# Performance work log

Hardware: AMD Instinct MI355X
Metric: run time of the kernel (lower is better)

## Reference

```python
import jax, jax.numpy as jnp
import numpy as np

B, T, C = 2, 2048, 2048
NH, NKV, HD = 16, 8, 256
SOFTCAP = 50.0
ROPE_BASE = 10000.0


def setup_inputs() -> dict:
    key = jax.random.key(0)
    ks = jax.random.split(key, 5)
    s = 0.02
    return {
        "X": jax.random.normal(ks[0], (B, T, C), dtype=jnp.float32),
        "Wq": jax.random.normal(ks[1], (C, NH * HD), dtype=jnp.float32) * s,
        "Wk": jax.random.normal(ks[2], (C, NKV * HD), dtype=jnp.float32) * s,
        "Wv": jax.random.normal(ks[3], (C, NKV * HD), dtype=jnp.float32) * s,
        "Wo": jax.random.normal(ks[4], (NH * HD, C), dtype=jnp.float32) * s,
    }


def _rotate_half(x):
    x1, x2 = x[..., : x.shape[-1] // 2], x[..., x.shape[-1] // 2 :]
    return jnp.concatenate((-x2, x1), axis=-1)


def _rope_cos_sin(t, head_dim, dtype):
    inv_freq = 1.0 / ROPE_BASE ** (
        jnp.arange(0, head_dim, 2, dtype=jnp.int32).astype(jnp.float32) / head_dim
    )  # [HD/2]
    pos = jnp.arange(t, dtype=jnp.float32)  # [T]
    freqs = pos[:, None] * inv_freq[None, :]  # [T, HD/2]
    emb = jnp.concatenate((freqs, freqs), axis=-1)  # [T, HD]
    # shape [1, 1, T, HD] to broadcast over (B, H, T, HD)
    return (
        jnp.cos(emb).astype(dtype)[None, None],
        jnp.sin(emb).astype(dtype)[None, None],
    )


def reference(X, Wq, Wk, Wv, Wo):
    b, t, c = X.shape
    n_rep = NH // NKV

    q = (X @ Wq).reshape(b, t, NH, HD).transpose(0, 2, 1, 3)   # [B,NH,T,HD]
    k = (X @ Wk).reshape(b, t, NKV, HD).transpose(0, 2, 1, 3)  # [B,NKV,T,HD]
    v = (X @ Wv).reshape(b, t, NKV, HD).transpose(0, 2, 1, 3)

    cos, sin = _rope_cos_sin(t, HD, X.dtype)
    q = q * cos + _rotate_half(q) * sin
    k = k * cos + _rotate_half(k) * sin

    # repeat_kv (GQA): [B,NKV,T,HD] -> [B,NH,T,HD]
    k = jnp.repeat(k, n_rep, axis=1)
    v = jnp.repeat(v, n_rep, axis=1)

    scale = 256.0 ** (-0.5)  # hardcoded in source
    att = jnp.einsum("bhqd,bhkd->bhqk", q, k) * scale
    # tanh logit softcapping
    att = SOFTCAP * jnp.tanh(att / SOFTCAP)
    # causal mask
    causal = jnp.tril(jnp.ones((t, t), dtype=bool))
    att = jnp.where(causal[None, None], att, -jnp.inf)
    att = jax.nn.softmax(att, axis=-1)

    y = jnp.einsum("bhqk,bhkd->bhqd", att, v)  # [B,NH,T,HD]
    y = y.transpose(0, 2, 1, 3).reshape(b, t, NH * HD)
    return y @ Wo
```

## Files before the change

### kernel.cpp

```cpp
#include <hip/hip_runtime.h>
#include <hip/hip_bf16.h>

#define NHD 16
#define NKVH 8
#define HDIM 256
#define TSEQ 2048
#define BATCH 2

typedef unsigned int   u32;
typedef unsigned short u16;

typedef __attribute__((ext_vector_type(8))) short bf16x8;
typedef __attribute__((ext_vector_type(4))) float floatx4;

__device__ inline u32 cvt2bf(float lo, float hi) {
  u32 r;
  asm("v_cvt_pk_bf16_f32 %0, %1, %2" : "=v"(r) : "v"(lo), "v"(hi));
  return r;
}
__device__ inline u16 f2bf(float f) {
  union { float f; u32 i; } v; v.f = f;
  u32 r = v.i + 0x7fffu + ((v.i >> 16) & 1u);
  return (u16)(r >> 16);
}
__device__ inline float bf2f(u16 u) {
  union { u32 i; float f; } v; v.i = ((u32)u) << 16; return v.f;
}
__device__ inline float fexp2(float x) {
  float r; asm("v_exp_f32 %0, %1" : "=v"(r) : "v"(x)); return r;
}
__device__ inline float frcp(float x) {
  float r; asm("v_rcp_f32 %0, %1" : "=v"(r) : "v"(x)); return r;
}

typedef const __attribute__((address_space(1))) u32* gptr_t;
typedef __attribute__((address_space(3))) u32* lptr_t;
__device__ inline void gl_lds16(const void* g, void* l) {
  __builtin_amdgcn_global_load_lds((gptr_t)g, (lptr_t)l, 16, 0, 0);
}

__device__ inline void tconv_body(const float* __restrict__ in,
                                  u16* __restrict__ out, int R, int Cc,
                                  int bx, int by, int tid) {
  __shared__ float tile[64][65];
  const int r0 = by * 64, c0 = bx * 64;
  const int tr = tid >> 4;
  const int tc = (tid & 15) * 4;
#pragma unroll
  for (int j = 0; j < 4; ++j) {
    float4 v = *(const float4*)(in + (size_t)(r0 + tr + j * 16) * Cc + c0 + tc);
    tile[tr + j * 16][tc + 0] = v.x;
    tile[tr + j * 16][tc + 1] = v.y;
    tile[tr + j * 16][tc + 2] = v.z;
    tile[tr + j * 16][tc + 3] = v.w;
  }
  __syncthreads();
#pragma unroll
  for (int j = 0; j < 4; ++j) {
    int c = tr + j * 16;
    u16 o[4];
#pragma unroll
    for (int i = 0; i < 4; ++i) o[i] = f2bf(tile[tc + i][c]);
    *(uint2*)(out + (size_t)(c0 + c) * R + r0 + tc) = *(const uint2*)o;
  }
}

__global__ __launch_bounds__(256) void tconv_k(
    const float* __restrict__ in, u16* __restrict__ out, int R, int Cc)
{
  tconv_body(in, out, R, Cc, blockIdx.x, blockIdx.y, threadIdx.x);
}

__global__ __launch_bounds__(256) void xconv_k(
    const float* __restrict__ in, u16* __restrict__ out)
{
  size_t i = (size_t)blockIdx.x * 256 + threadIdx.x;
  float4 a = *(const float4*)(in + i * 8);
  float4 b = *(const float4*)(in + i * 8 + 4);
  uint4 o;
  o.x = cvt2bf(a.x, a.y); o.y = cvt2bf(a.z, a.w);
  o.z = cvt2bf(b.x, b.y); o.w = cvt2bf(b.z, b.w);
  *(uint4*)(out + i * 8) = o;
}

__global__ __launch_bounds__(256) void prep_k(
    const float* __restrict__ X,  const float* __restrict__ Wq,
    const float* __restrict__ Wk, const float* __restrict__ Wv,
    u16* __restrict__ XB, u16* __restrict__ WqT, u16* __restrict__ WkvT)
{
  const int bid = blockIdx.x, tid = threadIdx.x;
  if (bid < 4096) {
    size_t i = (size_t)bid * 256 + tid;
    float4 a = *(const float4*)(X + i * 8);
    float4 b = *(const float4*)(X + i * 8 + 4);
    uint4 o;
    o.x = cvt2bf(a.x, a.y); o.y = cvt2bf(a.z, a.w);
    o.z = cvt2bf(b.x, b.y); o.w = cvt2bf(b.z, b.w);
    *(uint4*)(XB + i * 8) = o;
  } else if (bid < 6144) {
    int idx = bid - 4096;
    tconv_body(Wq, WqT, 2048, 4096, idx & 63, idx >> 6, tid);
  } else if (bid < 7168) {
    int idx = bid - 6144;
    tconv_body(Wk, WkvT, 2048, 2048, idx & 31, idx >> 5, tid);
  } else {
    int idx = bid - 7168;
    tconv_body(Wv, WkvT + (size_t)2048 * 2048, 2048, 2048, idx & 31, idx >> 5, tid);
  }
}

template<int EPI, int BM>
__global__ __launch_bounds__(512, 2) void gemm256_k(
    const u16* __restrict__ Ab, const u16* __restrict__ BTp,
    void* __restrict__ Op, int M, int N, int K)
{
  constexpr int NI = BM / 32;
  constexpr int AI = BM / 64;
  __shared__ u16 LA[2][BM * 64];
  __shared__ u16 LB[2][256 * 64];
  const int t = threadIdx.x;
  const int lane = t & 63, wave = t >> 6;
  const int lg = lane >> 4, l15 = lane & 15;
  const int wm = wave >> 2, wn = wave & 3;
  const int mtiles = M / BM;
  const int mt = (int)blockIdx.x % mtiles, nt = (int)blockIdx.x / mtiles;
  const int m0 = mt * BM, n0 = nt << 8;

  const int arow = wave * (BM / 8) + (lane >> 3);
  const int ska  = ((lane & 7) ^ (arow & 7)) << 3;
  const int brow = wave * 32 + (lane >> 3);
  const int skb  = ((lane & 7) ^ (brow & 7)) << 3;
  const u16* Ag = Ab  + (size_t)(m0 + arow) * K + ska;
  const u16* Bg = BTp + (size_t)(n0 + brow) * K + skb;

  auto STAGE = [&](int k0, int sel) {
#pragma unroll
    for (int q = 0; q < AI; ++q)
      gl_lds16(Ag + k0 + (size_t)q * 8 * K, &LA[sel][(wave * (BM / 8) + q * 8) * 64]);
#pragma unroll
    for (int q = 0; q < 4; ++q)
      gl_lds16(Bg + k0 + (size_t)q * 8 * K, &LB[sel][(wave * 32 + q * 8) * 64]);
  };

  floatx4 acc[NI][4];
#pragma unroll
  for (int i = 0; i < NI; ++i)
#pragma unroll
    for (int j = 0; j < 4; ++j) acc[i][j] = (floatx4){0.f, 0.f, 0.f, 0.f};

  STAGE(0, 0);
  const int KT = K >> 6;
  for (int kt = 0; kt < KT; ++kt) {
    const int sel = kt & 1;
    if (kt + 1 < KT) {
      STAGE((kt + 1) << 6, sel ^ 1);
      if constexpr (BM == 256) asm volatile("s_waitcnt vmcnt(8)" ::: "memory");
      else                     asm volatile("s_waitcnt vmcnt(6)" ::: "memory");
    } else {
      asm volatile("s_waitcnt vmcnt(0)" ::: "memory");
    }
    __builtin_amdgcn_s_barrier();
    __builtin_amdgcn_sched_barrier(0);
    __builtin_amdgcn_s_setprio(1);
#pragma unroll
    for (int ks = 0; ks < 2; ++ks) {
      const int c = (ks << 2) + lg;
      bf16x8 bfv[4];
#pragma unroll
      for (int j = 0; j < 4; ++j) {
        int row = wn * 64 + (j << 4) + l15;
        bfv[j] = *(const bf16x8*)(&LB[sel][row * 64 + ((c ^ (row & 7)) << 3)]);
      }
#pragma unroll
      for (int i = 0; i < NI; ++i) {
        int row = wm * (BM / 2) + (i << 4) + l15;
        bf16x8 af = *(const bf16x8*)(&LA[sel][row * 64 + ((c ^ (row & 7)) << 3)]);
#pragma unroll
        for (int j = 0; j < 4; ++j)
          acc[i][j] = __builtin_amdgcn_mfma_f32_16x16x32_bf16(af, bfv[j], acc[i][j], 0, 0, 0);
      }
    }
    __builtin_amdgcn_s_setprio(0);
    __builtin_amdgcn_s_barrier();
  }

#pragma unroll
  for (int i = 0; i < NI; ++i) {
#pragma unroll
    for (int j = 0; j < 4; ++j) {
#pragma unroll
      for (int r = 0; r < 4; ++r) {
        int m = m0 + wm * (BM / 2) + (i << 4) + (lg << 2) + r;
        int n = n0 + wn * 64 + (j << 4) + l15;
        float v = acc[i][j][r];
        int bb = m >> 11, tt = m & 2047;
        if (EPI == 0) {
          ((float*)Op)[(size_t)m * N + n] = v;
        } else if (EPI == 1) {
          int h = n >> 8, d = n & 255;
          ((u16*)Op)[(((size_t)bb * NHD + h) * TSEQ + tt) * HDIM + d] = f2bf(v);
        } else {
          if (n < 2048) {
            int h = n >> 8, d = n & 255;
            ((u16*)Op)[(((size_t)bb * NKVH + h) * TSEQ + tt) * HDIM + d] = f2bf(v);
          } else {
            int n2 = n - 2048;
            int h = n2 >> 8, d = n2 & 255;
            ((u16*)Op)[8388608u + (((size_t)bb * NKVH + h) * HDIM + d) * TSEQ + tt] = f2bf(v);
          }
        }
      }
    }
  }
}

__global__ __launch_bounds__(256) void rope_k(u16* Qb, u16* Kb) {
  size_t idx = (size_t)blockIdx.x * 256 + threadIdx.x;
  const size_t qtot = (size_t)BATCH * NHD * TSEQ * 128;
  u16* buf;
  if (idx < qtot) buf = Qb;
  else { idx -= qtot; buf = Kb; }
  int d = (int)(idx & 127);
  size_t rest = idx >> 7;
  int tt = (int)(rest & (TSEQ - 1));
  float invf = exp2f(-(float)d * 0.103810253f);
  float th = (float)tt * invf;
  float sn, cs;
  sincosf(th, &sn, &cs);
  size_t base = rest * HDIM;
  float x1 = bf2f(buf[base + d]);
  float x2 = bf2f(buf[base + d + 128]);
  buf[base + d]       = f2bf(x1 * cs - x2 * sn);
  buf[base + d + 128] = f2bf(x2 * cs + x1 * sn);
}

__global__ __launch_bounds__(256, 2) void attn_k(
    const u16* __restrict__ Q, const u16* __restrict__ Kb,
    const u16* __restrict__ Vt, u16* __restrict__ Y)
{
  __shared__ u16 Ks2[2][32 * 256];
  __shared__ u16 Vs2[2][256 * 32];
  __shared__ u16 Ps[4 * 16 * 32];
  __shared__ float Ls[4][16];
  const int t = threadIdx.x, lane = t & 63, w = t >> 6;
  const int lg = lane >> 4, l15 = lane & 15;
  const int qt = 31 - (int)blockIdx.y;
  const int h = (int)blockIdx.x >> 1, b = (int)blockIdx.x & 1;
  const int hkv = h >> 1;

  const u16* Kg = Kb + ((size_t)(b * NKVH + hkv)) * TSEQ * HDIM;
  const u16* Vg = Vt + ((size_t)(b * NKVH + hkv)) * HDIM * TSEQ;

  int koff[4], voff[4];
#pragma unroll
  for (int q = 0; q < 4; ++q) {
    int krow = w * 8 + q * 2 + (lane >> 5);
    int kcc  = lane & 31;
    koff[q] = krow * 256 + ((kcc ^ (krow & 7)) << 3);
    int vd  = w * 64 + q * 16 + (lane >> 2);
    voff[q] = vd * TSEQ + (((lane & 3) ^ ((vd >> 2) & 3)) << 3);
  }

  auto STAGE = [&](int st, int sel) {
    const u16* kbase = Kg + (size_t)st * (32 * 256);
    const u16* vbase = Vg + st * 32;
#pragma unroll
    for (int q = 0; q < 4; ++q)
      gl_lds16(kbase + koff[q], &Ks2[sel][(w * 8 + q * 2) * 256]);
#pragma unroll
    for (int q = 0; q < 4; ++q)
      gl_lds16(vbase + voff[q], &Vs2[sel][(w * 64 + q * 16) * 32]);
  };

  const u16* Qg = Q + (((size_t)(b * NHD + h)) * TSEQ + qt * 64 + w * 16 + l15) * HDIM;
  bf16x8 qf[8];
#pragma unroll
  for (int ks = 0; ks < 8; ++ks) qf[ks] = *(const bf16x8*)(Qg + ks * 32 + lg * 8);

  floatx4 accY[16];
#pragma unroll
  for (int i = 0; i < 16; ++i) accY[i] = (floatx4){0.f, 0.f, 0.f, 0.f};
  float rsum = 0.f;

  const int qglob = qt * 64 + w * 16 + l15;
  const int qmaxw = qt * 64 + w * 16 + 15;
  const int nst = 2 * qt + 2;
  const int fps = (l15 ^ (l15 >> 2)) & 3;

  STAGE(0, 0);
  for (int st = 0; st < nst; ++st) {
    const int sel = st & 1;
    if (st + 1 < nst) {
      STAGE(st + 1, sel ^ 1);
      asm volatile("s_waitcnt vmcnt(8)" ::: "memory");
    } else {
      asm volatile("s_waitcnt vmcnt(0)" ::: "memory");
    }
    __builtin_amdgcn_s_barrier();
    __builtin_amdgcn_sched_barrier(0);

    if (st * 32 <= qmaxw) {
      __builtin_amdgcn_s_setprio(1);
#pragma unroll
      for (int stile = 0; stile < 2; ++stile) {
        floatx4 sa0 = (floatx4){0.f, 0.f, 0.f, 0.f};
        floatx4 sa1 = (floatx4){0.f, 0.f, 0.f, 0.f};
#pragma unroll
        for (int ks = 0; ks < 8; ++ks) {
          int row = (stile << 4) + l15;
          int c = (ks << 2) + lg;
          bf16x8 kf = *(const bf16x8*)((const char*)Ks2[sel] +
                        row * 512 + ((c ^ (row & 7)) << 4));
          if (ks & 1)
            sa1 = __builtin_amdgcn_mfma_f32_16x16x32_bf16(kf, qf[ks], sa1, 0, 0, 0);
          else
            sa0 = __builtin_amdgcn_mfma_f32_16x16x32_bf16(kf, qf[ks], sa0, 0, 0, 0);
        }
        int sbase = st * 32 + (stile << 4) + (lg << 2);
        float p[4];
#pragma unroll
        for (int r = 0; r < 4; ++r) {
          float u = fexp2((sa0[r] + sa1[r]) * 0.0036067376f);
          float pv = fexp2(-144.26950408f * frcp(u + 1.0f));
          pv = (sbase + r <= qglob) ? pv : 0.0f;
          p[r] = pv;
          rsum += pv;
        }
        uint2 pw;
        pw.x = cvt2bf(p[0], p[1]);
        pw.y = cvt2bf(p[2], p[3]);
        int o = (stile << 5) + (lg << 3);
        int gran = (o >> 4) ^ fps;
        *(uint2*)((char*)Ps + (w << 10) + l15 * 64 + (gran << 4) + (o & 15)) = pw;
      }
      {
        bf16x8 pf = *(const bf16x8*)((const char*)Ps + (w << 10) + l15 * 64 +
                      ((lg ^ fps) << 4));
#pragma unroll
        for (int dt = 0; dt < 16; ++dt) {
          int row = (dt << 4) + l15;
          bf16x8 vf = *(const bf16x8*)((const char*)Vs2[sel] +
                        row * 64 + ((lg ^ ((row >> 2) & 3)) << 4));
          accY[dt] = __builtin_amdgcn_mfma_f32_16x16x32_bf16(pf, vf, accY[dt], 0, 0, 0);
        }
      }
      __builtin_amdgcn_s_setprio(0);
    }
    __builtin_amdgcn_s_barrier();
  }

  rsum += __shfl_xor(rsum, 16);
  rsum += __shfl_xor(rsum, 32);
  if (lane < 16) Ls[w][l15] = rsum;
  __syncthreads();
  float inv[4];
#pragma unroll
  for (int r = 0; r < 4; ++r) inv[r] = 1.0f / Ls[w][(lg << 2) + r];

  u16* Yg = Y + ((size_t)(b * TSEQ + qt * 64 + w * 16)) * (NHD * HDIM) + h * HDIM;
#pragma unroll
  for (int dt = 0; dt < 16; ++dt)
#pragma unroll
    for (int r = 0; r < 4; ++r)
      Yg[(size_t)((lg << 2) + r) * (NHD * HDIM) + (dt << 4) + l15] =
          f2bf(accY[dt][r] * inv[r]);
}

extern "C" void kernel_launch(void* const* d_in, const int* in_sizes, int n_in,
                              void* d_out, int out_size, void* d_ws, size_t ws_size,
                              hipStream_t stream) {
  const float* X  = (const float*)d_in[0];
  const float* Wq = (const float*)d_in[1];
  const float* Wk = (const float*)d_in[2];
  const float* Wv = (const float*)d_in[3];
  const float* Wo = (const float*)d_in[4];
  float* out = (float*)d_out;

  u16* ws = (u16*)d_ws;
  dim3 blk(256);

  if (ws_size >= (size_t)117440512) {
    u16* XB   = ws;
    u16* WqT  = ws + 8388608;
    u16* WkvT = ws + 16777216;
    u16* Qb   = ws + 25165824;
    u16* KVb  = ws + 41943040;
    u16* Yb   = ws;
    u16* WoT  = ws + 25165824;

    prep_k<<<dim3(8192), blk, 0, stream>>>(X, Wq, Wk, Wv, XB, WqT, WkvT);
    gemm256_k<1, 256><<<dim3(256), dim3(512), 0, stream>>>(XB, WqT,  Qb,  4096, 4096, 2048);
    gemm256_k<3, 256><<<dim3(256), dim3(512), 0, stream>>>(XB, WkvT, KVb, 4096, 4096, 2048);
    rope_k<<<dim3(49152), blk, 0, stream>>>(Qb, KVb);
    attn_k<<<dim3(32, 32), blk, 0, stream>>>(Qb, KVb, KVb + 8388608, Yb);
    tconv_k<<<dim3(32, 64), blk, 0, stream>>>(Wo, WoT, 4096, 2048);
    gemm256_k<0, 128><<<dim3(256), dim3(512), 0, stream>>>(Yb, WoT, out, 4096, 2048, 4096);
  } else {
    u16* XB   = ws;
    u16* WT   = ws + 8388608;
    u16* Qb   = ws + 16777216;
    u16* KVb  = ws + 33554432;
    u16* Yb   = ws;
    u16* WoT  = ws + 16777216;

    xconv_k<<<dim3(4096), blk, 0, stream>>>(X, XB);
    tconv_k<<<dim3(64, 32), blk, 0, stream>>>(Wq, WT, 2048, 4096);
    gemm256_k<1, 256><<<dim3(256), dim3(512), 0, stream>>>(XB, WT, Qb, 4096, 4096, 2048);
    tconv_k<<<dim3(32, 32), blk, 0, stream>>>(Wk, WT, 2048, 2048);
    tconv_k<<<dim3(32, 32), blk, 0, stream>>>(Wv, WT + (size_t)2048 * 2048, 2048, 2048);
    gemm256_k<3, 256><<<dim3(256), dim3(512), 0, stream>>>(XB, WT, KVb, 4096, 4096, 2048);
    rope_k<<<dim3(49152), blk, 0, stream>>>(Qb, KVb);
    attn_k<<<dim3(32, 32), blk, 0, stream>>>(Qb, KVb, KVb + 8388608, Yb);
    tconv_k<<<dim3(32, 64), blk, 0, stream>>>(Wo, WoT, 4096, 2048);
    gemm256_k<0, 128><<<dim3(256), dim3(512), 0, stream>>>(Yb, WoT, out, 4096, 2048, 4096);
  }
}
```

Baseline: 421.6 us.

## Process 128 query rows per attention block to reuse K/V tiles

Each wave now computes two 16-row query groups against every staged K/V tile, doubling the query tile per block and halving the grid. This halves global and LDS staging traffic of K/V per query row and reuses each K/V fragment read from LDS across two MFMAs. The cost is doubled accumulator registers, which risks spilling, and coarser causal work units with fewer blocks, which can hurt load balance.

```diff
diff --git a/kernel.cpp b/kernel.cpp
--- a/kernel.cpp
+++ b/kernel.cpp
@@ -234,17 +234,18 @@
   buf[base + d + 128] = f2bf(x2 * cs + x1 * sn);
 }
 
-__global__ __launch_bounds__(256, 2) void attn_k(
+__global__ __attribute__((amdgpu_waves_per_eu(2, 2))) __launch_bounds__(256)
+void attn_k(
     const u16* __restrict__ Q, const u16* __restrict__ Kb,
     const u16* __restrict__ Vt, u16* __restrict__ Y)
 {
   __shared__ u16 Ks2[2][32 * 256];
   __shared__ u16 Vs2[2][256 * 32];
-  __shared__ u16 Ps[4 * 16 * 32];
-  __shared__ float Ls[4][16];
+  __shared__ u16 Ps[4 * 32 * 32];
+  __shared__ float Ls[4][2][16];
   const int t = threadIdx.x, lane = t & 63, w = t >> 6;
   const int lg = lane >> 4, l15 = lane & 15;
-  const int qt = 31 - (int)blockIdx.y;
+  const int qt = 15 - (int)blockIdx.y;
   const int h = (int)blockIdx.x >> 1, b = (int)blockIdx.x & 1;
   const int hkv = h >> 1;
 
@@ -272,19 +273,27 @@
       gl_lds16(vbase + voff[q], &Vs2[sel][(w * 64 + q * 16) * 32]);
   };
 
-  const u16* Qg = Q + (((size_t)(b * NHD + h)) * TSEQ + qt * 64 + w * 16 + l15) * HDIM;
-  bf16x8 qf[8];
-#pragma unroll
-  for (int ks = 0; ks < 8; ++ks) qf[ks] = *(const bf16x8*)(Qg + ks * 32 + lg * 8);
-
-  floatx4 accY[16];
-#pragma unroll
-  for (int i = 0; i < 16; ++i) accY[i] = (floatx4){0.f, 0.f, 0.f, 0.f};
-  float rsum = 0.f;
-
-  const int qglob = qt * 64 + w * 16 + l15;
-  const int qmaxw = qt * 64 + w * 16 + 15;
-  const int nst = 2 * qt + 2;
+  bf16x8 qf[2][8];
+#pragma unroll
+  for (int g = 0; g < 2; ++g) {
+    const u16* Qg = Q + (((size_t)(b * NHD + h)) * TSEQ +
+                         qt * 128 + w * 32 + g * 16 + l15) * HDIM;
+#pragma unroll
+    for (int ks = 0; ks < 8; ++ks)
+      qf[g][ks] = *(const bf16x8*)(Qg + ks * 32 + lg * 8);
+  }
+
+  floatx4 accY[2][16];
+#pragma unroll
+  for (int g = 0; g < 2; ++g)
+#pragma unroll
+    for (int i = 0; i < 16; ++i) accY[g][i] = (floatx4){0.f, 0.f, 0.f, 0.f};
+  float rsum0 = 0.f, rsum1 = 0.f;
+
+  const int qg0 = qt * 128 + w * 32 + l15;
+  const int qg1 = qg0 + 16;
+  const int qmaxw = qt * 128 + w * 32 + 31;
+  const int nst = 4 * qt + 4;
   const int fps = (l15 ^ (l15 >> 2)) & 3;
 
   STAGE(0, 0);
@@ -306,42 +315,64 @@
         floatx4 sa0 = (floatx4){0.f, 0.f, 0.f, 0.f};
         floatx4 sa1 = (floatx4){0.f, 0.f, 0.f, 0.f};
 #pragma unroll
-        for (int ks = 0; ks < 8; ++ks) {
-          int row = (stile << 4) + l15;
-          int c = (ks << 2) + lg;
-          bf16x8 kf = *(const bf16x8*)((const char*)Ks2[sel] +
-                        row * 512 + ((c ^ (row & 7)) << 4));
-          if (ks & 1)
-            sa1 = __builtin_amdgcn_mfma_f32_16x16x32_bf16(kf, qf[ks], sa1, 0, 0, 0);
-          else
-            sa0 = __builtin_amdgcn_mfma_f32_16x16x32_bf16(kf, qf[ks], sa0, 0, 0, 0);
+        for (int kh = 0; kh < 2; ++kh) {
+          bf16x8 kf[4];
+#pragma unroll
+          for (int kk = 0; kk < 4; ++kk) {
+            int ks = kh * 4 + kk;
+            int row = (stile << 4) + l15;
+            int c = (ks << 2) + lg;
+            kf[kk] = *(const bf16x8*)((const char*)Ks2[sel] +
+                       row * 512 + ((c ^ (row & 7)) << 4));
+          }
+#pragma unroll
+          for (int kk = 0; kk < 4; ++kk) {
+            sa0 = __builtin_amdgcn_mfma_f32_16x16x32_bf16(kf[kk], qf[0][kh * 4 + kk], sa0, 0, 0, 0);
+            sa1 = __builtin_amdgcn_mfma_f32_16x16x32_bf16(kf[kk], qf[1][kh * 4 + kk], sa1, 0, 0, 0);
+          }
         }
         int sbase = st * 32 + (stile << 4) + (lg << 2);
-        float p[4];
-#pragma unroll
-        for (int r = 0; r < 4; ++r) {
-          float u = fexp2((sa0[r] + sa1[r]) * 0.0036067376f);
-          float pv = fexp2(-144.26950408f * frcp(u + 1.0f));
-          pv = (sbase + r <= qglob) ? pv : 0.0f;
-          p[r] = pv;
-          rsum += pv;
-        }
-        uint2 pw;
-        pw.x = cvt2bf(p[0], p[1]);
-        pw.y = cvt2bf(p[2], p[3]);
         int o = (stile << 5) + (lg << 3);
         int gran = (o >> 4) ^ fps;
-        *(uint2*)((char*)Ps + (w << 10) + l15 * 64 + (gran << 4) + (o & 15)) = pw;
+        {
+          float p[4];
+#pragma unroll
+          for (int r = 0; r < 4; ++r) {
+            float u = fexp2(sa0[r] * 0.0036067376f);
+            float pv = fexp2(-144.26950408f * frcp(u + 1.0f));
+            pv = (sbase + r <= qg0) ? pv : 0.0f;
+            p[r] = pv;
+            rsum0 += pv;
+          }
+          uint2 pw; pw.x = cvt2bf(p[0], p[1]); pw.y = cvt2bf(p[2], p[3]);
+          *(uint2*)((char*)Ps + (w << 11) + l15 * 64 + (gran << 4) + (o & 15)) = pw;
+        }
+        {
+          float p[4];
+#pragma unroll
+          for (int r = 0; r < 4; ++r) {
+            float u = fexp2(sa1[r] * 0.0036067376f);
+            float pv = fexp2(-144.26950408f * frcp(u + 1.0f));
+            pv = (sbase + r <= qg1) ? pv : 0.0f;
+            p[r] = pv;
+            rsum1 += pv;
+          }
+          uint2 pw; pw.x = cvt2bf(p[0], p[1]); pw.y = cvt2bf(p[2], p[3]);
+          *(uint2*)((char*)Ps + (w << 11) + (16 + l15) * 64 + (gran << 4) + (o & 15)) = pw;
+        }
       }
       {
-        bf16x8 pf = *(const bf16x8*)((const char*)Ps + (w << 10) + l15 * 64 +
-                      ((lg ^ fps) << 4));
+        bf16x8 pf0 = *(const bf16x8*)((const char*)Ps + (w << 11) +
+                       l15 * 64 + ((lg ^ fps) << 4));
+        bf16x8 pf1 = *(const bf16x8*)((const char*)Ps + (w << 11) +
+                       (16 + l15) * 64 + ((lg ^ fps) << 4));
 #pragma unroll
         for (int dt = 0; dt < 16; ++dt) {
           int row = (dt << 4) + l15;
           bf16x8 vf = *(const bf16x8*)((const char*)Vs2[sel] +
                         row * 64 + ((lg ^ ((row >> 2) & 3)) << 4));
-          accY[dt] = __builtin_amdgcn_mfma_f32_16x16x32_bf16(pf, vf, accY[dt], 0, 0, 0);
+          accY[0][dt] = __builtin_amdgcn_mfma_f32_16x16x32_bf16(pf0, vf, accY[0][dt], 0, 0, 0);
+          accY[1][dt] = __builtin_amdgcn_mfma_f32_16x16x32_bf16(pf1, vf, accY[1][dt], 0, 0, 0);
         }
       }
       __builtin_amdgcn_s_setprio(0);
@@ -349,21 +380,26 @@
     __builtin_amdgcn_s_barrier();
   }
 
-  rsum += __shfl_xor(rsum, 16);
-  rsum += __shfl_xor(rsum, 32);
-  if (lane < 16) Ls[w][l15] = rsum;
+  rsum0 += __shfl_xor(rsum0, 16);
+  rsum0 += __shfl_xor(rsum0, 32);
+  rsum1 += __shfl_xor(rsum1, 16);
+  rsum1 += __shfl_xor(rsum1, 32);
+  if (lane < 16) { Ls[w][0][l15] = rsum0; Ls[w][1][l15] = rsum1; }
   __syncthreads();
-  float inv[4];
-#pragma unroll
-  for (int r = 0; r < 4; ++r) inv[r] = 1.0f / Ls[w][(lg << 2) + r];
-
-  u16* Yg = Y + ((size_t)(b * TSEQ + qt * 64 + w * 16)) * (NHD * HDIM) + h * HDIM;
-#pragma unroll
-  for (int dt = 0; dt < 16; ++dt)
-#pragma unroll
-    for (int r = 0; r < 4; ++r)
-      Yg[(size_t)((lg << 2) + r) * (NHD * HDIM) + (dt << 4) + l15] =
-          f2bf(accY[dt][r] * inv[r]);
+#pragma unroll
+  for (int g = 0; g < 2; ++g) {
+    float inv[4];
+#pragma unroll
+    for (int r = 0; r < 4; ++r) inv[r] = 1.0f / Ls[w][g][(lg << 2) + r];
+    u16* Yg = Y + ((size_t)(b * TSEQ + qt * 128 + w * 32 + g * 16)) * (NHD * HDIM) +
+              h * HDIM;
+#pragma unroll
+    for (int dt = 0; dt < 16; ++dt)
+#pragma unroll
+      for (int r = 0; r < 4; ++r)
+        Yg[(size_t)((lg << 2) + r) * (NHD * HDIM) + (dt << 4) + l15] =
+            f2bf(accY[g][dt][r] * inv[r]);
+  }
 }
 
 extern "C" void kernel_launch(void* const* d_in, const int* in_sizes, int n_in,
@@ -392,7 +428,7 @@
     gemm256_k<1, 256><<<dim3(256), dim3(512), 0, stream>>>(XB, WqT,  Qb,  4096, 4096, 2048);
     gemm256_k<3, 256><<<dim3(256), dim3(512), 0, stream>>>(XB, WkvT, KVb, 4096, 4096, 2048);
     rope_k<<<dim3(49152), blk, 0, stream>>>(Qb, KVb);
-    attn_k<<<dim3(32, 32), blk, 0, stream>>>(Qb, KVb, KVb + 8388608, Yb);
+    attn_k<<<dim3(32, 16), blk, 0, stream>>>(Qb, KVb, KVb + 8388608, Yb);
     tconv_k<<<dim3(32, 64), blk, 0, stream>>>(Wo, WoT, 4096, 2048);
     gemm256_k<0, 128><<<dim3(256), dim3(512), 0, stream>>>(Yb, WoT, out, 4096, 2048, 4096);
   } else {
@@ -410,7 +446,7 @@
     tconv_k<<<dim3(32, 32), blk, 0, stream>>>(Wv, WT + (size_t)2048 * 2048, 2048, 2048);
     gemm256_k<3, 256><<<dim3(256), dim3(512), 0, stream>>>(XB, WT, KVb, 4096, 4096, 2048);
     rope_k<<<dim3(49152), blk, 0, stream>>>(Qb, KVb);
-    attn_k<<<dim3(32, 32), blk, 0, stream>>>(Qb, KVb, KVb + 8388608, Yb);
+    attn_k<<<dim3(32, 16), blk, 0, stream>>>(Qb, KVb, KVb + 8388608, Yb);
     tconv_k<<<dim3(32, 64), blk, 0, stream>>>(Wo, WoT, 4096, 2048);
     gemm256_k<0, 128><<<dim3(256), dim3(512), 0, stream>>>(Yb, WoT, out, 4096, 2048, 4096);
   }
```

Result: slower. 518.1 us (+22.9%).
